# Optimization experiments

Hardware: AMD Instinct MI355X
Metric: run time of the kernel (lower is better)

The kernel has to match this reference:

```python
import jax, jax.numpy as jnp
import numpy as np

N_EXPERTS = 8
TOP_K = 2
D_MODEL = 1024
N_TOKENS = 8192


def setup_inputs() -> dict:
    key = jax.random.key(0)
    k1, k2, k3, k4, k5 = jax.random.split(key, 5)
    x = jax.random.normal(k1, (N_TOKENS, D_MODEL), dtype=jnp.float32)
    # router Linear(num_experts): weight [d, E], bias [E]
    Wr = jax.random.normal(k2, (D_MODEL, N_EXPERTS), dtype=jnp.float32) / np.sqrt(D_MODEL)
    br = jnp.zeros((N_EXPERTS,), dtype=jnp.float32)
    # per-expert Linear(d_model): stacked weights [E, d, d], biases [E, d]
    W = jax.random.normal(k3, (N_EXPERTS, D_MODEL, D_MODEL), dtype=jnp.float32) / np.sqrt(D_MODEL)
    b = jnp.zeros((N_EXPERTS, D_MODEL), dtype=jnp.float32)
    return {"x": x, "Wr": Wr, "br": br, "W": W, "b": b}


def reference(x, Wr, br, W, b):
    # --- route ---
    logits = x @ Wr + br                                  # [N, E]
    top_k_vals, top_k_idxs = jax.lax.top_k(logits, TOP_K)  # [N, k]
    top_k_gates = jax.nn.softmax(top_k_vals, axis=-1)      # [N, k]
    # --- experts (dense form of gather-dispatch; same math as routed compute) ---
    y_all = jnp.einsum('nd,edh->neh', x, W) + b            # [N, E, d]
    # --- gather routed expert outputs per slot ---
    y_k = jnp.take_along_axis(y_all, top_k_idxs[:, :, None], axis=1)  # [N, k, d]
    # --- weighted scatter-combine (reduce) ---
    out = jnp.sum(top_k_gates[:, :, None] * y_k, axis=1)   # [N, d]
    return out
```

## Files before the change

kernel.cpp:

```cpp
#include <hip/hip_runtime.h>
#include <hip/hip_bf16.h>


#define NTOK 8192
#define DM   1024
#define NEXP 8
#define CAP  8192
#define MAXT 136

#define RTB  512
#define TRB2 256

typedef __attribute__((ext_vector_type(8))) short bf16x8;
typedef __attribute__((ext_vector_type(4))) float f32x4;

__device__ __forceinline__ unsigned short f2bf(float f) {
  unsigned u = __float_as_uint(f);
  unsigned r = (u + 0x7fffu + ((u >> 16) & 1u)) >> 16;
  return (unsigned short)r;
}
__device__ __forceinline__ float bf2f(unsigned short s) {
  return __uint_as_float(((unsigned)s) << 16);
}

__device__ __forceinline__ void gl_lds16(const void* g, void* l) {
  __builtin_amdgcn_global_load_lds(
      (const __attribute__((address_space(1))) unsigned int*)g,
      (__attribute__((address_space(3))) unsigned int*)l, 16, 0, 0);
}

__global__ __launch_bounds__(256) void prep_kernel(
    const float* __restrict__ W, unsigned short* __restrict__ Wt,
    const float* __restrict__ x, const float* __restrict__ Wr,
    const float* __restrict__ br, unsigned short* __restrict__ xbf,
    int4* __restrict__ topk, int* __restrict__ counts,
    int* __restrict__ tok, int2* __restrict__ pos,
    int* __restrict__ done, int* __restrict__ desc,
    int* __restrict__ ntiles, int* __restrict__ offset) {
  __shared__ __align__(16) unsigned int smem4[16384];
  const int tid = threadIdx.x;

  if (blockIdx.x >= RTB) {
    const int tb = blockIdx.x - RTB;
    const int e = tb >> 5;
    const int rem = tb & 31;
    const int D0 = (rem >> 3) * 256;
    const int H0 = (rem & 7) * 128;
    const int dp = tid >> 5;
    const int c  = tid & 31;

    const float* Wsrc = W + (size_t)e * DM * DM + (size_t)D0 * DM + H0 + c * 4;
#pragma unroll 4
    for (int i = 0; i < 16; i++) {
      const int dc = dp + 8 * i;
      const int d = dc * 2;
      float4 a = *(const float4*)(Wsrc + (size_t)d * DM);
      float4 b = *(const float4*)(Wsrc + (size_t)(d + 1) * DM);
      unsigned pk[4];
      pk[0] = (unsigned)f2bf(a.x) | ((unsigned)f2bf(b.x) << 16);
      pk[1] = (unsigned)f2bf(a.y) | ((unsigned)f2bf(b.y) << 16);
      pk[2] = (unsigned)f2bf(a.z) | ((unsigned)f2bf(b.z) << 16);
      pk[3] = (unsigned)f2bf(a.w) | ((unsigned)f2bf(b.w) << 16);
#pragma unroll
      for (int j = 0; j < 4; j++) {
        const int h = c * 4 + j;
        const int pg = (dc >> 2) ^ (h >> 2);
        smem4[h * 128 + pg * 4 + (dc & 3)] = pk[j];
      }
    }
    __syncthreads();

    const int hp = tid >> 5;
    const int ch = tid & 31;
    unsigned short* Wdst =
        Wt + (size_t)e * DM * DM + (size_t)H0 * DM + D0;
#pragma unroll 4
    for (int o = 0; o < 16; o++) {
      const int h = hp + 8 * o;
      const int pg = ch ^ (h >> 2);
      uint4 v = *(const uint4*)(smem4 + h * 128 + pg * 4);
      *(uint4*)(Wdst + (size_t)h * DM + ch * 8) = v;
    }
    return;
  }

  int*  lcnt  = (int*)smem4;
  int4* ltop  = (int4*)(smem4 + 8);
  int2* lrank = (int2*)(smem4 + 72);

  const int rb = blockIdx.x;
  const int wave = tid >> 6, lane = tid & 63;
  const int tb = rb * 16 + wave * 4;
  if (tid < NEXP) lcnt[tid] = 0;

  const int c0 = lane * 16;
  const float* wr = Wr + (size_t)c0 * NEXP;
  const float* xr = x + (size_t)tb * DM + c0;

  float v[4][16];
#pragma unroll
  for (int tt = 0; tt < 4; tt++) {
#pragma unroll
    for (int i = 0; i < 4; i++) {
      float4 f = *(const float4*)(xr + (size_t)tt * DM + i * 4);
      v[tt][i * 4 + 0] = f.x; v[tt][i * 4 + 1] = f.y;
      v[tt][i * 4 + 2] = f.z; v[tt][i * 4 + 3] = f.w;
    }
  }
#pragma unroll
  for (int tt = 0; tt < 4; tt++) {
    union { unsigned short s[8]; uint4 q; } pk;
#pragma unroll
    for (int half = 0; half < 2; half++) {
#pragma unroll
      for (int i = 0; i < 8; i++) pk.s[i] = f2bf(v[tt][half * 8 + i]);
      *(uint4*)(xbf + (size_t)(tb + tt) * DM + c0 + half * 8) = pk.q;
    }
  }
  float p[4][8] = {};
#pragma unroll
  for (int i = 0; i < 16; i++) {
    float4 wl = *(const float4*)(wr + i * 8);
    float4 wh = *(const float4*)(wr + i * 8 + 4);
#pragma unroll
    for (int tt = 0; tt < 4; tt++) {
      float xv = v[tt][i];
      p[tt][0] += xv * wl.x; p[tt][1] += xv * wl.y;
      p[tt][2] += xv * wl.z; p[tt][3] += xv * wl.w;
      p[tt][4] += xv * wh.x; p[tt][5] += xv * wh.y;
      p[tt][6] += xv * wh.z; p[tt][7] += xv * wh.w;
    }
  }
#pragma unroll
  for (int off = 32; off >= 1; off >>= 1) {
#pragma unroll
    for (int tt = 0; tt < 4; tt++)
#pragma unroll
      for (int e = 0; e < 8; e++)
        p[tt][e] += __shfl_xor(p[tt][e], off, 64);
  }
  if (lane == 0) {
#pragma unroll
    for (int tt = 0; tt < 4; tt++) {
      float lg[8];
#pragma unroll
      for (int e = 0; e < 8; e++) lg[e] = p[tt][e] + br[e];
      float v0 = lg[0]; int i0 = 0;
#pragma unroll
      for (int e = 1; e < 8; e++) if (lg[e] > v0) { v0 = lg[e]; i0 = e; }
      float v1 = -3.4e38f; int i1 = 0;
#pragma unroll
      for (int e = 0; e < 8; e++)
        if (e != i0 && lg[e] > v1) { v1 = lg[e]; i1 = e; }
      float ee = __expf(v1 - v0);
      float g0 = 1.0f / (1.0f + ee);
      float g1 = ee / (1.0f + ee);
      int4 rec;
      rec.x = i0; rec.y = i1;
      rec.z = __float_as_int(g0); rec.w = __float_as_int(g1);
      ltop[wave * 4 + tt] = rec;
      topk[tb + tt] = rec;
    }
  }
  __syncthreads();

  if (tid < 16) {
    int4 r = ltop[tid];
    int s0 = atomicAdd(&lcnt[r.x], 1);
    int s1 = atomicAdd(&lcnt[r.y], 1);
    int2 rk; rk.x = s0; rk.y = s1;
    lrank[tid] = rk;
  }
  __syncthreads();
  if (tid < NEXP) lcnt[tid] = atomicAdd(&counts[tid], lcnt[tid]);
  __syncthreads();
  if (tid < 16) {
    int4 r = ltop[tid];
    int2 rk = lrank[tid];
    int p0 = lcnt[r.x] + rk.x;
    int p1 = lcnt[r.y] + rk.y;
    int t = rb * 16 + tid;
    tok[r.x * CAP + p0] = t;
    tok[r.y * CAP + p1] = t;
    int2 pr; pr.x = p0; pr.y = p1;
    pos[t] = pr;
  }
  __syncthreads();

  if (tid == 0) {
    __threadfence();
    if (atomicAdd(done, 1) == RTB - 1) {
      __threadfence();
      int cnt[NEXP];
#pragma unroll
      for (int e = 0; e < NEXP; e++) cnt[e] = atomicAdd(&counts[e], 0);
      int idx = 0, off = 0;
#pragma unroll
      for (int e = 0; e < NEXP; e++) {
        offset[e] = off;
        off += cnt[e];
        int nm = (cnt[e] + 127) >> 7;
        for (int i = 0; i < nm; i++) desc[idx++] = (e << 16) | i;
      }
      *ntiles = idx;
    }
  }
}

__global__ __launch_bounds__(256) void moe_gemm_kernel(
    const unsigned short* __restrict__ xbf, const unsigned short* __restrict__ wt,
    const int* __restrict__ counts, const int* __restrict__ offset,
    const int* __restrict__ tok, const int* __restrict__ desc,
    const int* __restrict__ ntiles, unsigned short* __restrict__ ybuf) {
  const int slot = blockIdx.y;
  if (slot >= *ntiles) return;
  const int dsc = desc[slot];
  const int e = dsc >> 16;
  const int m0 = (dsc & 0xffff) * 128;
  const int cnt = counts[e];
  const int n0 = blockIdx.x * 128;

  __shared__ __align__(16) unsigned short sA0[128 * 32];
  __shared__ __align__(16) unsigned short sB0[128 * 32];
  __shared__ __align__(16) unsigned short sA1[128 * 32];
  __shared__ __align__(16) unsigned short sB1[128 * 32];
  __shared__ int sTok[128];

  const int tid = threadIdx.x, wave = tid >> 6, lane = tid & 63;

  if (tid < 128) {
    int sr = m0 + tid;
    int cl = (sr < cnt) ? sr : (cnt - 1);
    sTok[tid] = tok[e * CAP + cl];
  }
  __syncthreads();

  const int rA1 = wave * 16 + (lane >> 2);
  const int rA2 = rA1 + 64;
  const int cch = lane & 3;
  const int cg1 = (cch ^ ((rA1 >> 1) & 3)) * 8;
  const int cg2 = (cch ^ ((rA2 >> 1) & 3)) * 8;
  const unsigned short* pA1 = xbf + (size_t)sTok[rA1] * DM + cg1;
  const unsigned short* pA2 = xbf + (size_t)sTok[rA2] * DM + cg2;
  const unsigned short* wte = wt + (size_t)e * DM * DM;
  const unsigned short* pB1 = wte + (size_t)(n0 + rA1) * DM + cg1;
  const unsigned short* pB2 = wte + (size_t)(n0 + rA2) * DM + cg2;
  const int lo1 = wave * 512, lo2 = (wave + 4) * 512;

  const int q = lane >> 4, ml = lane & 15;
  const int wm = (wave >> 1) * 64, wn = (wave & 1) * 64;
  int offA[4], offB[4];
#pragma unroll
  for (int i = 0; i < 4; i++) {
    int row = wm + i * 16 + ml;
    offA[i] = row * 32 + (q ^ ((row >> 1) & 3)) * 8;
    int rowb = wn + i * 16 + ml;
    offB[i] = rowb * 32 + (q ^ ((rowb >> 1) & 3)) * 8;
  }

  f32x4 acc[4][4] = {};

  for (int k0 = 0; k0 < DM; k0 += 64) {
    gl_lds16(pA1 + k0, sA0 + lo1);
    gl_lds16(pA2 + k0, sA0 + lo2);
    gl_lds16(pB1 + k0, sB0 + lo1);
    gl_lds16(pB2 + k0, sB0 + lo2);
    gl_lds16(pA1 + k0 + 32, sA1 + lo1);
    gl_lds16(pA2 + k0 + 32, sA1 + lo2);
    gl_lds16(pB1 + k0 + 32, sB1 + lo1);
    gl_lds16(pB2 + k0 + 32, sB1 + lo2);
    __syncthreads();
    bf16x8 af0[4], bf0[4], af1[4], bf1[4];
#pragma unroll
    for (int i = 0; i < 4; i++) {
      af0[i] = *(const bf16x8*)(sA0 + offA[i]);
      bf0[i] = *(const bf16x8*)(sB0 + offB[i]);
      af1[i] = *(const bf16x8*)(sA1 + offA[i]);
      bf1[i] = *(const bf16x8*)(sB1 + offB[i]);
    }
#pragma unroll
    for (int mt = 0; mt < 4; mt++)
#pragma unroll
      for (int nt = 0; nt < 4; nt++)
        acc[mt][nt] = __builtin_amdgcn_mfma_f32_16x16x32_bf16(
            af0[mt], bf0[nt], acc[mt][nt], 0, 0, 0);
#pragma unroll
    for (int mt = 0; mt < 4; mt++)
#pragma unroll
      for (int nt = 0; nt < 4; nt++)
        acc[mt][nt] = __builtin_amdgcn_mfma_f32_16x16x32_bf16(
            af1[mt], bf1[nt], acc[mt][nt], 0, 0, 0);
    __syncthreads();
  }

  const int yb = offset[e] + m0;
#pragma unroll
  for (int mt = 0; mt < 4; mt++) {
    int rbase = wm + mt * 16 + q * 4;
#pragma unroll
    for (int r = 0; r < 4; r++) {
      int row = rbase + r;
      if (m0 + row >= cnt) continue;
      unsigned short* yrow = ybuf + (size_t)(yb + row) * DM + n0;
#pragma unroll
      for (int nt = 0; nt < 4; nt++) {
        yrow[wn + nt * 16 + ml] = f2bf(acc[mt][nt][r]);
      }
    }
  }
}

__global__ __launch_bounds__(256) void combine_kernel(
    const unsigned short* __restrict__ ybuf, const int4* __restrict__ topk,
    const int2* __restrict__ pos, const int* __restrict__ offset,
    const float* __restrict__ bias, float* __restrict__ out) {
  const int c = threadIdx.x * 4;
  const int t0 = blockIdx.x * 4;
#pragma unroll
  for (int i = 0; i < 4; i++) {
    const int t = t0 + i;
    int4 r = topk[t];
    int2 p = pos[t];
    float g0 = __int_as_float(r.z), g1 = __int_as_float(r.w);
    int s0 = offset[r.x] + p.x;
    int s1 = offset[r.y] + p.y;
    ushort4 ya = *(const ushort4*)(ybuf + (size_t)s0 * DM + c);
    ushort4 yb = *(const ushort4*)(ybuf + (size_t)s1 * DM + c);
    float4 b0 = *(const float4*)(bias + (size_t)r.x * DM + c);
    float4 b1 = *(const float4*)(bias + (size_t)r.y * DM + c);
    float4 o;
    o.x = g0 * (bf2f(ya.x) + b0.x) + g1 * (bf2f(yb.x) + b1.x);
    o.y = g0 * (bf2f(ya.y) + b0.y) + g1 * (bf2f(yb.y) + b1.y);
    o.z = g0 * (bf2f(ya.z) + b0.z) + g1 * (bf2f(yb.z) + b1.z);
    o.w = g0 * (bf2f(ya.w) + b0.w) + g1 * (bf2f(yb.w) + b1.w);
    *(float4*)(out + (size_t)t * DM + c) = o;
  }
}

extern "C" void kernel_launch(void* const* d_in, const int* in_sizes, int n_in,
                              void* d_out, int out_size, void* d_ws, size_t ws_size,
                              hipStream_t stream) {
  const float* x  = (const float*)d_in[0];
  const float* Wr = (const float*)d_in[1];
  const float* br = (const float*)d_in[2];
  const float* W  = (const float*)d_in[3];
  const float* b  = (const float*)d_in[4];
  float* out = (float*)d_out;

  char* ws = (char*)d_ws;
  unsigned short* xbf  = (unsigned short*)ws;
  unsigned short* wt   = (unsigned short*)(ws + (16u << 20));
  unsigned short* ybuf = (unsigned short*)(ws + (32u << 20));
  char* ctrl = ws + (64u << 20);
  int*   counts = (int*)ctrl;
  int*   ntiles = (int*)(ctrl + 64);
  int*   done   = (int*)(ctrl + 96);
  int*   offset = (int*)(ctrl + 128);
  int*   desc   = (int*)(ctrl + 256);
  int*   tok    = (int*)(ctrl + 4096);
  int2*  pos    = (int2*)(ctrl + 4096 + (256u << 10));
  int4*  topk   = (int4*)(ctrl + 4096 + (320u << 10));

  hipMemsetAsync(ctrl, 0, 128, stream);

  prep_kernel<<<RTB + TRB2, 256, 0, stream>>>(
      W, wt, x, Wr, br, xbf, topk, counts, tok, pos, done, desc, ntiles, offset);
  moe_gemm_kernel<<<dim3(8, MAXT), 256, 0, stream>>>(
      xbf, wt, counts, offset, tok, desc, ntiles, ybuf);
  combine_kernel<<<NTOK / 4, 256, 0, stream>>>(ybuf, topk, pos, offset, b, out);
}
```

Measured before the change: 206.2 us.

## Split prep kernel into separate router and weight-cast kernels with smaller tiles

The fused prep kernel, which carried a 64KB shared buffer for every block including router blocks, is split into a router kernel using only tiny shared arrays and a separate weight transpose/cast kernel. The router now handles 2 tokens per wave with coalesced lane-strided loads over 1024 blocks. The weight cast uses 128x128 tiles with 32KB LDS over 512 blocks. This aims to raise occupancy and improve coalescing, at the cost of an extra kernel launch and losing the overlap between routing and weight conversion.

```diff
diff --git a/kernel.cpp b/kernel.cpp
--- a/kernel.cpp
+++ b/kernel.cpp
@@ -8,8 +8,8 @@
 #define CAP  8192
 #define MAXT 136
 
-#define RTB  512
-#define TRB2 256
+#define RBLK 1024
+#define WBLK 512
 
 typedef __attribute__((ext_vector_type(8))) short bf16x8;
 typedef __attribute__((ext_vector_type(4))) float f32x4;
@@ -29,119 +29,75 @@
       (__attribute__((address_space(3))) unsigned int*)l, 16, 0, 0);
 }
 
-__global__ __launch_bounds__(256) void prep_kernel(
-    const float* __restrict__ W, unsigned short* __restrict__ Wt,
+__global__ __launch_bounds__(256) void router_kernel(
     const float* __restrict__ x, const float* __restrict__ Wr,
     const float* __restrict__ br, unsigned short* __restrict__ xbf,
     int4* __restrict__ topk, int* __restrict__ counts,
     int* __restrict__ tok, int2* __restrict__ pos,
     int* __restrict__ done, int* __restrict__ desc,
     int* __restrict__ ntiles, int* __restrict__ offset) {
-  __shared__ __align__(16) unsigned int smem4[16384];
+  __shared__ int lcnt[NEXP];
+  __shared__ int4 ltop[8];
+  __shared__ int2 lrank[8];
   const int tid = threadIdx.x;
-
-  if (blockIdx.x >= RTB) {
-    const int tb = blockIdx.x - RTB;
-    const int e = tb >> 5;
-    const int rem = tb & 31;
-    const int D0 = (rem >> 3) * 256;
-    const int H0 = (rem & 7) * 128;
-    const int dp = tid >> 5;
-    const int c  = tid & 31;
-
-    const float* Wsrc = W + (size_t)e * DM * DM + (size_t)D0 * DM + H0 + c * 4;
-#pragma unroll 4
-    for (int i = 0; i < 16; i++) {
-      const int dc = dp + 8 * i;
-      const int d = dc * 2;
-      float4 a = *(const float4*)(Wsrc + (size_t)d * DM);
-      float4 b = *(const float4*)(Wsrc + (size_t)(d + 1) * DM);
-      unsigned pk[4];
-      pk[0] = (unsigned)f2bf(a.x) | ((unsigned)f2bf(b.x) << 16);
-      pk[1] = (unsigned)f2bf(a.y) | ((unsigned)f2bf(b.y) << 16);
-      pk[2] = (unsigned)f2bf(a.z) | ((unsigned)f2bf(b.z) << 16);
-      pk[3] = (unsigned)f2bf(a.w) | ((unsigned)f2bf(b.w) << 16);
-#pragma unroll
-      for (int j = 0; j < 4; j++) {
-        const int h = c * 4 + j;
-        const int pg = (dc >> 2) ^ (h >> 2);
-        smem4[h * 128 + pg * 4 + (dc & 3)] = pk[j];
-      }
-    }
-    __syncthreads();
-
-    const int hp = tid >> 5;
-    const int ch = tid & 31;
-    unsigned short* Wdst =
-        Wt + (size_t)e * DM * DM + (size_t)H0 * DM + D0;
-#pragma unroll 4
-    for (int o = 0; o < 16; o++) {
-      const int h = hp + 8 * o;
-      const int pg = ch ^ (h >> 2);
-      uint4 v = *(const uint4*)(smem4 + h * 128 + pg * 4);
-      *(uint4*)(Wdst + (size_t)h * DM + ch * 8) = v;
-    }
-    return;
-  }
-
-  int*  lcnt  = (int*)smem4;
-  int4* ltop  = (int4*)(smem4 + 8);
-  int2* lrank = (int2*)(smem4 + 72);
-
   const int rb = blockIdx.x;
   const int wave = tid >> 6, lane = tid & 63;
-  const int tb = rb * 16 + wave * 4;
+  const int tb = rb * 8 + wave * 2;
   if (tid < NEXP) lcnt[tid] = 0;
 
-  const int c0 = lane * 16;
-  const float* wr = Wr + (size_t)c0 * NEXP;
-  const float* xr = x + (size_t)tb * DM + c0;
-
-  float v[4][16];
-#pragma unroll
-  for (int tt = 0; tt < 4; tt++) {
+  const int l4 = lane * 4;
+
+  float v[2][16];
+#pragma unroll
+  for (int tt = 0; tt < 2; tt++) {
 #pragma unroll
     for (int i = 0; i < 4; i++) {
-      float4 f = *(const float4*)(xr + (size_t)tt * DM + i * 4);
+      float4 f = *(const float4*)(x + (size_t)(tb + tt) * DM + i * 256 + l4);
       v[tt][i * 4 + 0] = f.x; v[tt][i * 4 + 1] = f.y;
       v[tt][i * 4 + 2] = f.z; v[tt][i * 4 + 3] = f.w;
     }
   }
 #pragma unroll
-  for (int tt = 0; tt < 4; tt++) {
-    union { unsigned short s[8]; uint4 q; } pk;
-#pragma unroll
-    for (int half = 0; half < 2; half++) {
-#pragma unroll
-      for (int i = 0; i < 8; i++) pk.s[i] = f2bf(v[tt][half * 8 + i]);
-      *(uint4*)(xbf + (size_t)(tb + tt) * DM + c0 + half * 8) = pk.q;
-    }
-  }
-  float p[4][8] = {};
-#pragma unroll
-  for (int i = 0; i < 16; i++) {
-    float4 wl = *(const float4*)(wr + i * 8);
-    float4 wh = *(const float4*)(wr + i * 8 + 4);
-#pragma unroll
-    for (int tt = 0; tt < 4; tt++) {
-      float xv = v[tt][i];
-      p[tt][0] += xv * wl.x; p[tt][1] += xv * wl.y;
-      p[tt][2] += xv * wl.z; p[tt][3] += xv * wl.w;
-      p[tt][4] += xv * wh.x; p[tt][5] += xv * wh.y;
-      p[tt][6] += xv * wh.z; p[tt][7] += xv * wh.w;
+  for (int tt = 0; tt < 2; tt++) {
+#pragma unroll
+    for (int i = 0; i < 4; i++) {
+      uint2 pk;
+      pk.x = (unsigned)f2bf(v[tt][i * 4 + 0]) |
+             ((unsigned)f2bf(v[tt][i * 4 + 1]) << 16);
+      pk.y = (unsigned)f2bf(v[tt][i * 4 + 2]) |
+             ((unsigned)f2bf(v[tt][i * 4 + 3]) << 16);
+      *(uint2*)(xbf + (size_t)(tb + tt) * DM + i * 256 + l4) = pk;
+    }
+  }
+  float p[2][8] = {};
+#pragma unroll
+  for (int i = 0; i < 4; i++) {
+#pragma unroll
+    for (int j = 0; j < 4; j++) {
+      const float* wrow = Wr + (size_t)(i * 256 + l4 + j) * NEXP;
+      float4 wl = *(const float4*)(wrow);
+      float4 wh = *(const float4*)(wrow + 4);
+#pragma unroll
+      for (int tt = 0; tt < 2; tt++) {
+        float xv = v[tt][i * 4 + j];
+        p[tt][0] += xv * wl.x; p[tt][1] += xv * wl.y;
+        p[tt][2] += xv * wl.z; p[tt][3] += xv * wl.w;
+        p[tt][4] += xv * wh.x; p[tt][5] += xv * wh.y;
+        p[tt][6] += xv * wh.z; p[tt][7] += xv * wh.w;
+      }
     }
   }
 #pragma unroll
   for (int off = 32; off >= 1; off >>= 1) {
 #pragma unroll
-    for (int tt = 0; tt < 4; tt++)
+    for (int tt = 0; tt < 2; tt++)
 #pragma unroll
       for (int e = 0; e < 8; e++)
         p[tt][e] += __shfl_xor(p[tt][e], off, 64);
   }
   if (lane == 0) {
 #pragma unroll
-    for (int tt = 0; tt < 4; tt++) {
+    for (int tt = 0; tt < 2; tt++) {
       float lg[8];
 #pragma unroll
       for (int e = 0; e < 8; e++) lg[e] = p[tt][e] + br[e];
@@ -158,13 +114,13 @@
       int4 rec;
       rec.x = i0; rec.y = i1;
       rec.z = __float_as_int(g0); rec.w = __float_as_int(g1);
-      ltop[wave * 4 + tt] = rec;
+      ltop[wave * 2 + tt] = rec;
       topk[tb + tt] = rec;
     }
   }
   __syncthreads();
 
-  if (tid < 16) {
+  if (tid < 8) {
     int4 r = ltop[tid];
     int s0 = atomicAdd(&lcnt[r.x], 1);
     int s1 = atomicAdd(&lcnt[r.y], 1);
@@ -174,12 +130,12 @@
   __syncthreads();
   if (tid < NEXP) lcnt[tid] = atomicAdd(&counts[tid], lcnt[tid]);
   __syncthreads();
-  if (tid < 16) {
+  if (tid < 8) {
     int4 r = ltop[tid];
     int2 rk = lrank[tid];
     int p0 = lcnt[r.x] + rk.x;
     int p1 = lcnt[r.y] + rk.y;
-    int t = rb * 16 + tid;
+    int t = rb * 8 + tid;
     tok[r.x * CAP + p0] = t;
     tok[r.y * CAP + p1] = t;
     int2 pr; pr.x = p0; pr.y = p1;
@@ -189,7 +145,7 @@
 
   if (tid == 0) {
     __threadfence();
-    if (atomicAdd(done, 1) == RTB - 1) {
+    if (atomicAdd(done, 1) == RBLK - 1) {
       __threadfence();
       int cnt[NEXP];
 #pragma unroll
@@ -204,6 +160,51 @@
       }
       *ntiles = idx;
     }
+  }
+}
+
+__global__ __launch_bounds__(256) void wcast_kernel(
+    const float* __restrict__ W, unsigned short* __restrict__ Wt) {
+  __shared__ __align__(16) unsigned int smem[8192];
+  const int tid = threadIdx.x;
+  const int tb = blockIdx.x;
+  const int e = tb >> 6;
+  const int rem = tb & 63;
+  const int D0 = (rem >> 3) * 128;
+  const int H0 = (rem & 7) * 128;
+
+  const int dp = tid >> 5;
+  const int c  = tid & 31;
+  const float* Wsrc = W + (size_t)e * DM * DM + (size_t)D0 * DM + H0 + c * 4;
+#pragma unroll 4
+  for (int i = 0; i < 8; i++) {
+    const int dc = dp + 8 * i;
+    const int d = dc * 2;
+    float4 a = *(const float4*)(Wsrc + (size_t)d * DM);
+    float4 b = *(const float4*)(Wsrc + (size_t)(d + 1) * DM);
+    unsigned pk[4];
+    pk[0] = (unsigned)f2bf(a.x) | ((unsigned)f2bf(b.x) << 16);
+    pk[1] = (unsigned)f2bf(a.y) | ((unsigned)f2bf(b.y) << 16);
+    pk[2] = (unsigned)f2bf(a.z) | ((unsigned)f2bf(b.z) << 16);
+    pk[3] = (unsigned)f2bf(a.w) | ((unsigned)f2bf(b.w) << 16);
+#pragma unroll
+    for (int j = 0; j < 4; j++) {
+      const int h = c * 4 + j;
+      const int pg = ((dc >> 2) ^ (h >> 2)) & 15;
+      smem[h * 64 + pg * 4 + (dc & 3)] = pk[j];
+    }
+  }
+  __syncthreads();
+
+  const int hh = tid >> 4;
+  const int g  = tid & 15;
+  unsigned short* Wdst = Wt + (size_t)e * DM * DM + (size_t)H0 * DM + D0;
+#pragma unroll 4
+  for (int o = 0; o < 8; o++) {
+    const int h = hh + 16 * o;
+    const int pg = (g ^ (h >> 2)) & 15;
+    uint4 v = *(const uint4*)(smem + h * 64 + pg * 4);
+    *(uint4*)(Wdst + (size_t)h * DM + g * 8) = v;
   }
 }
 
@@ -363,8 +364,9 @@
 
   hipMemsetAsync(ctrl, 0, 128, stream);
 
-  prep_kernel<<<RTB + TRB2, 256, 0, stream>>>(
-      W, wt, x, Wr, br, xbf, topk, counts, tok, pos, done, desc, ntiles, offset);
+  router_kernel<<<RBLK, 256, 0, stream>>>(
+      x, Wr, br, xbf, topk, counts, tok, pos, done, desc, ntiles, offset);
+  wcast_kernel<<<WBLK, 256, 0, stream>>>(W, wt);
   moe_gemm_kernel<<<dim3(8, MAXT), 256, 0, stream>>>(
       xbf, wt, counts, offset, tok, desc, ntiles, ybuf);
   combine_kernel<<<NTOK / 4, 256, 0, stream>>>(ybuf, topk, pos, offset, b, out);
```

Measured after the change: 225.7 us. 9.5% more time.
